# Optimization experiments

Hardware: AMD Instinct MI355X
Metric: run time of the kernel (lower is better)

The kernel has to match this reference:

```python
import jax, jax.numpy as jnp
import numpy as np

D_MODEL = 1024
N_HEADS = 16
N_KV_HEADS = 4
HEAD_DIM = D_MODEL // N_HEADS
GROUP = N_HEADS // N_KV_HEADS
ROPE_BASE = 10000.0


def _rope(x):
    # x: (B, H, T, Dh); standard rotate-half RoPE, base 10000
    B, H, T, Dh = x.shape
    inv_freq = 1.0 / (ROPE_BASE ** (jnp.arange(0, Dh, 2, dtype=jnp.float32) / Dh))
    t = jnp.arange(T, dtype=jnp.float32)
    freqs = t[:, None] * inv_freq[None, :]              # (T, Dh/2)
    emb = jnp.concatenate([freqs, freqs], axis=-1)      # (T, Dh)
    cos = jnp.cos(emb)[None, None].astype(x.dtype)
    sin = jnp.sin(emb)[None, None].astype(x.dtype)
    x1, x2 = x[..., : Dh // 2], x[..., Dh // 2 :]
    rot = jnp.concatenate([-x2, x1], axis=-1)
    return x * cos + rot * sin


def setup_inputs() -> dict:
    key = jax.random.key(0)
    ks = jax.random.split(key, 5)
    B, T = 2, 2048
    s = 1.0 / np.sqrt(D_MODEL)
    return {
        "x": jax.random.normal(ks[0], (B, T, D_MODEL), dtype=jnp.float32),
        "wq": jax.random.normal(ks[1], (D_MODEL, N_HEADS * HEAD_DIM), dtype=jnp.float32) * s,
        "wk": jax.random.normal(ks[2], (D_MODEL, N_KV_HEADS * HEAD_DIM), dtype=jnp.float32) * s,
        "wv": jax.random.normal(ks[3], (D_MODEL, N_KV_HEADS * HEAD_DIM), dtype=jnp.float32) * s,
        "wo": jax.random.normal(ks[4], (N_HEADS * HEAD_DIM, D_MODEL), dtype=jnp.float32) * s,
    }


def reference(x, wq, wk, wv, wo):
    B, T, _ = x.shape
    q = (x @ wq).reshape(B, T, N_HEADS, HEAD_DIM).transpose(0, 2, 1, 3)      # (B,H,T,Dh)
    k = (x @ wk).reshape(B, T, N_KV_HEADS, HEAD_DIM).transpose(0, 2, 1, 3)   # (B,Hk,T,Dh)
    v = (x @ wv).reshape(B, T, N_KV_HEADS, HEAD_DIM).transpose(0, 2, 1, 3)
    q = _rope(q)
    k = _rope(k)
    # repeat_interleave kv heads group_size times -> (B, H, T, Dh)
    k = jnp.repeat(k, GROUP, axis=1)
    v = jnp.repeat(v, GROUP, axis=1)
    scale = 1.0 / np.sqrt(HEAD_DIM)
    scores = jnp.einsum("bhqd,bhkd->bhqk", q, k) * scale                      # (B,H,T,T)
    causal = jnp.tril(jnp.ones((T, T), dtype=bool))
    scores = jnp.where(causal[None, None], scores, -jnp.inf)
    attn = jax.nn.softmax(scores, axis=-1)
    out = jnp.einsum("bhqk,bhkd->bhqd", attn, v)                              # (B,H,T,Dh)
    out = out.transpose(0, 2, 1, 3).reshape(B, T, N_HEADS * HEAD_DIM)
    return out @ wo
```

## Files before the change

kernel.cpp:

```cpp
#include <hip/hip_runtime.h>

typedef short bshort8 __attribute__((ext_vector_type(8)));
typedef float f32x4 __attribute__((ext_vector_type(4)));

#define DEVFN static __device__ __forceinline__

DEVFN unsigned short f2bf(float f) {
    union { float f; unsigned u; } v; v.f = f;
    unsigned r = (v.u + 0x7FFFu + ((v.u >> 16) & 1u)) >> 16;
    return (unsigned short)r;
}

DEVFN float bf2f(unsigned short u) {
    union { unsigned u; float f; } v; v.u = (unsigned)u << 16;
    return v.f;
}

DEVFN unsigned cvt_pk_bf16(float a, float b) {
    unsigned r;
    asm("v_cvt_pk_bf16_f32 %0, %1, %2" : "=v"(r) : "v"(a), "v"(b));
    return r;
}

DEVFN float exp2_fast(float x) {
    float r;
    asm("v_exp_f32 %0, %1" : "=v"(r) : "v"(x));
    return r;
}

DEVFN int swzf(int row) { return (row & 7) ^ ((row >> 3) & 7); }
DEVFN int swzf2(int row) { return (row & 3) ^ ((row >> 2) & 3); }

#define GLDS16(g, l)                                                            \
    __builtin_amdgcn_global_load_lds(                                           \
        (__attribute__((address_space(1))) void*)(g),                           \
        (__attribute__((address_space(3))) void*)(l), 16, 0, 0)

__global__ void prep_kernel(const float* __restrict__ x,
                            const float* __restrict__ wq,
                            const float* __restrict__ wk,
                            const float* __restrict__ wv,
                            const float* __restrict__ wo,
                            unsigned short* __restrict__ xb,
                            unsigned short* __restrict__ wt,
                            unsigned short* __restrict__ wot,
                            float2* __restrict__ cs) {
    const int z = blockIdx.z;
    int tx = threadIdx.x, ty = threadIdx.y;
    if (z >= 5) {
        int i = ((z - 5) * 1024 + blockIdx.y * 32 + blockIdx.x) * 256 + ty * 32 + tx;
        float4 v = ((const float4*)x)[i];
        ushort4 o;
        o.x = f2bf(v.x); o.y = f2bf(v.y); o.z = f2bf(v.z); o.w = f2bf(v.w);
        ((ushort4*)xb)[i] = o;
        return;
    }
    if (z == 4) {
        int idx = (blockIdx.y * 32 + blockIdx.x) * 256 + ty * 32 + tx;
        if (idx < 65536) {
            int t = idx >> 5, i = idx & 31;
            float inv_freq = powf(10000.0f, -(float)i / 32.0f);
            float a = (float)t * inv_freq;
            cs[idx] = make_float2(cosf(a), sinf(a));
        }
        return;
    }
    const float* src;
    unsigned short* dst;
    int N;
    if (z == 0)      { src = wq; dst = wt;                N = 1024; }
    else if (z == 1) { src = wk; dst = wt + 1024 * 1024;  N = 256; }
    else if (z == 2) { src = wv; dst = wt + 1280 * 1024;  N = 256; }
    else             { src = wo; dst = wot;               N = 1024; }
    if (blockIdx.x * 32 >= N) return;
    __shared__ float tile[32][33];
    int n0 = blockIdx.x * 32, k0 = blockIdx.y * 32;
#pragma unroll
    for (int i = 0; i < 4; i++)
        tile[ty + i * 8][tx] = src[(size_t)(k0 + ty + i * 8) * N + n0 + tx];
    __syncthreads();
#pragma unroll
    for (int i = 0; i < 4; i++)
        dst[(size_t)(n0 + ty + i * 8) * 1024 + k0 + tx] = f2bf(tile[tx][ty + i * 8]);
}


__global__ __launch_bounds__(256) void gemm_qkv_kernel(
    const unsigned short* __restrict__ xb, const unsigned short* __restrict__ wt,
    const float2* __restrict__ cs, unsigned short* __restrict__ Qb,
    unsigned short* __restrict__ Kb, unsigned short* __restrict__ Vt) {
    __shared__ char smem[49152];
    const int tid = threadIdx.x;
    const int lane = tid & 63, w = tid >> 6;
    const int m0 = blockIdx.y * 128, n0 = blockIdx.x * 64;
    const int l15 = lane & 15, g = lane >> 4;
    const int l8 = lane >> 3, c8 = lane & 7;

    const unsigned short* srcA[4];
    int dstA[4];
#pragma unroll
    for (int j = 0; j < 4; j++) {
        int row = w * 32 + j * 8 + l8;
        srcA[j] = xb + (size_t)(m0 + row) * 1024 + (c8 ^ swzf(row)) * 8;
        dstA[j] = w * 4096 + j * 1024 + lane * 16;
    }
    const unsigned short* srcB[2];
    int dstB[2];
#pragma unroll
    for (int j = 0; j < 2; j++) {
        int row = w * 16 + j * 8 + l8;
        srcB[j] = wt + (size_t)(n0 + row) * 1024 + (c8 ^ swzf(row)) * 8;
        dstB[j] = 0x8000 + w * 2048 + j * 1024 + lane * 16;
    }

    int aOff[2][2], bOff[4][2];
#pragma unroll
    for (int fm = 0; fm < 2; fm++) {
        int row = w * 32 + fm * 16 + l15;
#pragma unroll
        for (int ks = 0; ks < 2; ks++)
            aOff[fm][ks] = row * 128 + (((ks * 4 + g) ^ swzf(row)) << 4);
    }
#pragma unroll
    for (int fn = 0; fn < 4; fn++) {
        int row = fn * 16 + l15;
#pragma unroll
        for (int ks = 0; ks < 2; ks++)
            bOff[fn][ks] = row * 128 + (((ks * 4 + g) ^ swzf(row)) << 4);
    }

    f32x4 acc[2][4] = {};
#pragma unroll
    for (int j = 0; j < 4; j++) GLDS16(srcA[j], smem + dstA[j]);
#pragma unroll
    for (int j = 0; j < 2; j++) GLDS16(srcB[j], smem + dstB[j]);
    asm volatile("s_waitcnt vmcnt(0)" ::: "memory");
    __builtin_amdgcn_s_barrier();

    for (int kt = 0; kt < 16; kt++) {
        const int curA = (kt & 1) << 14;
        const int curB = (kt & 1) << 13;
        if (kt < 15) {
            const int nA = curA ^ 0x4000, nB = curB ^ 0x2000;
#pragma unroll
            for (int j = 0; j < 4; j++)
                GLDS16(srcA[j] + (kt + 1) * 64, smem + nA + dstA[j]);
#pragma unroll
            for (int j = 0; j < 2; j++)
                GLDS16(srcB[j] + (kt + 1) * 64, smem + nB + dstB[j]);
        }
        bshort8 af[2][2], bf[4][2];
#pragma unroll
        for (int fm = 0; fm < 2; fm++)
#pragma unroll
            for (int ks = 0; ks < 2; ks++)
                af[fm][ks] = *(const bshort8*)(smem + curA + aOff[fm][ks]);
#pragma unroll
        for (int fn = 0; fn < 4; fn++)
#pragma unroll
            for (int ks = 0; ks < 2; ks++)
                bf[fn][ks] = *(const bshort8*)(smem + 0x8000 + curB + bOff[fn][ks]);
        asm volatile("s_waitcnt lgkmcnt(0)" ::: "memory");
        __builtin_amdgcn_sched_barrier(0);
#pragma unroll
        for (int fm = 0; fm < 2; fm++)
#pragma unroll
            for (int fn = 0; fn < 4; fn++) {
                acc[fm][fn] = __builtin_amdgcn_mfma_f32_16x16x32_bf16(
                    af[fm][0], bf[fn][0], acc[fm][fn], 0, 0, 0);
                acc[fm][fn] = __builtin_amdgcn_mfma_f32_16x16x32_bf16(
                    af[fm][1], bf[fn][1], acc[fm][fn], 0, 0, 0);
            }
        if (kt < 15) {
            asm volatile("s_waitcnt vmcnt(0)" ::: "memory");
            __builtin_amdgcn_s_barrier();
        }
    }

    const bool isV = (n0 >= 1280);
    const bool isK = (n0 >= 1024) && !isV;
#pragma unroll
    for (int fm = 0; fm < 2; fm++) {
#pragma unroll
        for (int r = 0; r < 4; r++) {
            int m = m0 + w * 32 + fm * 16 + g * 4 + r;
            int b = m >> 11, t = m & 2047;
            if (isV) {
#pragma unroll
                for (int fn = 0; fn < 4; fn++) {
                    int n = n0 + fn * 16 + l15;
                    int d = n & 63, vh = (n - 1280) >> 6;
                    Vt[((size_t)(b * 4 + vh) * 64 + d) * 2048 + t] =
                        f2bf(acc[fm][fn][r]);
                }
            } else {
                float2 c0 = cs[t * 32 + l15];
                float2 c1 = cs[t * 32 + 16 + l15];
#pragma unroll
                for (int fn = 0; fn < 4; fn++) {
                    int n = n0 + fn * 16 + l15;
                    int d = n & 63;
                    float val = acc[fm][fn][r];
                    float pair = acc[fm][fn ^ 2][r];
                    float rot = (fn < 2) ? -pair : pair;
                    float2 cc = (fn & 1) ? c1 : c0;
                    float o = val * cc.x + rot * cc.y;
                    if (isK) {
                        int kh = (n - 1024) >> 6;
                        Kb[((size_t)(b * 4 + kh) * 2048 + t) * 64 + d] = f2bf(o);
                    } else {
                        o *= 0.1803368801111504f;
                        int h = n >> 6;
                        Qb[((size_t)(b * 16 + h) * 2048 + t) * 64 + d] = f2bf(o);
                    }
                }
            }
        }
    }
}


__global__ __launch_bounds__(256) void attn_kernel(
    const unsigned short* __restrict__ Qb, const unsigned short* __restrict__ Kb,
    const unsigned short* __restrict__ Vt, unsigned short* __restrict__ Opart,
    float* __restrict__ ml) {
    __shared__ char smem[24576];
    const int tid = threadIdx.x, lane = tid & 63, w = tid >> 6;
    const int l15 = lane & 15, g = lane >> 4;
    const int id = blockIdx.x;
    const int grp = id & 7;
    const int b = grp >> 2, kvh = grp & 3;
    const int i = id >> 3;
    const int hh = i & 3;
    const int h = kvh * 4 + hh;
    const int c = 79 - (i >> 2);
    int qt, s;
    if (c < 8)       { qt = c;                    s = 0; }
    else if (c < 24) { qt = 8 + ((c - 8) >> 1);   s = (c - 8) & 1; }
    else if (c < 48) { qt = 16 + (c - 24) / 3;    s = (c - 24) % 3; }
    else             { qt = 24 + ((c - 48) >> 2); s = (c - 48) & 3; }
    const int k0t = s * 8;
    const int nk = min(8, qt + 1 - k0t);
    const int qs = qt * 64;
    const int slot = (b * 16 + h) * 80 + c;

    const unsigned short* Kbase = Kb + (size_t)(b * 4 + kvh) * 2048 * 64;
    const unsigned short* Vbase = Vt + (size_t)(b * 4 + kvh) * 64 * 2048;
    const unsigned short* Qhead = Qb + (size_t)(b * 16 + h) * 2048 * 64;

    const int srow8 = lane >> 3;
    const int sci = lane & 7;
    const int sk = (l15 & 7) ^ (l15 >> 3);
    const int strip = w * 2048;

    const int rowb = l15 * 128 + ((g ^ sk) << 4);
    int Akn[4];
#pragma unroll
    for (int fn = 0; fn < 4; fn++) {
        int nr = ((fn >> 1) << 5) + ((l15 >> 2) << 3) + ((fn & 1) << 2) + (l15 & 3);
        int key = (nr & 7) ^ ((nr >> 3) & 1);
        Akn[fn] = nr * 128 + ((g ^ key) << 4);
    }

    const int lc0 = sci ^ srow8;
    const int lc1 = sci ^ srow8 ^ 1;
    const int r0 = w * 16 + srow8, r1 = w * 16 + 8 + srow8;
    const int kdst = strip + lane * 16;
    const int vdst0 = 0x2000 + strip + lane * 16;

    const unsigned short* Qrow = Qhead + (size_t)(qs + w * 16 + l15) * 64 + g * 8;
    bshort8 qf0 = *(const bshort8*)(Qrow);
    bshort8 qf1 = *(const bshort8*)(Qrow + 32);

    GLDS16(Kbase + (size_t)(k0t * 64 + r0) * 64 + lc0 * 8, smem + kdst);
    GLDS16(Kbase + (size_t)(k0t * 64 + r1) * 64 + lc1 * 8, smem + kdst + 1024);
    GLDS16(Vbase + (size_t)r0 * 2048 + k0t * 64 + lc0 * 8, smem + vdst0);
    GLDS16(Vbase + (size_t)r1 * 2048 + k0t * 64 + lc1 * 8, smem + vdst0 + 1024);
    __syncthreads();

    bshort8 ones;
#pragma unroll
    for (int j = 0; j < 8; j++) ones[j] = (short)0x3F80;

    const unsigned short* gk0 = Kbase + (size_t)((k0t + 1) * 64 + r0) * 64 + lc0 * 8;
    const unsigned short* gk1 = Kbase + (size_t)((k0t + 1) * 64 + r1) * 64 + lc1 * 8;
    const unsigned short* gv0 = Vbase + (size_t)r0 * 2048 + (k0t + 1) * 64 + lc0 * 8;
    const unsigned short* gv1 = Vbase + (size_t)r1 * 2048 + (k0t + 1) * 64 + lc1 * 8;

    f32x4 l_acc = {};
    f32x4 O[4] = {};
    const int qlocal = w * 16 + l15;
    const bool has_diag = (k0t + nk - 1 == qt);

    auto body = [&](int kt, bool more) {
        const int vb = (kt & 1) ? 0x4000 : 0x2000;
        const int vnb = (kt & 1) ? 0x2000 : 0x4000;
        if (more) {
            GLDS16(gv0 + kt * 64, smem + vnb + strip + lane * 16);
            GLDS16(gv1 + kt * 64, smem + vnb + strip + lane * 16 + 1024);
        }
        f32x4 S[4];
        __builtin_amdgcn_s_setprio(1);
#pragma unroll
        for (int fn = 0; fn < 4; fn++) {
            bshort8 k0 = *(const bshort8*)(smem + Akn[fn]);
            bshort8 k1 = *(const bshort8*)(smem + (Akn[fn] ^ 0x40));
            f32x4 a = {};
            a = __builtin_amdgcn_mfma_f32_16x16x32_bf16(k0, qf0, a, 0, 0, 0);
            a = __builtin_amdgcn_mfma_f32_16x16x32_bf16(k1, qf1, a, 0, 0, 0);
            S[fn] = a;
        }
        __builtin_amdgcn_s_setprio(0);
        __builtin_amdgcn_s_barrier();
        if (more) {
            GLDS16(gk0 + (size_t)kt * 4096, smem + kdst);
            GLDS16(gk1 + (size_t)kt * 4096, smem + kdst + 1024);
        }
        if (has_diag && !more) {
#pragma unroll
            for (int fn = 0; fn < 4; fn++)
#pragma unroll
                for (int r = 0; r < 4; r++) {
                    int kvl = ((fn >> 1) << 5) + (g << 3) + ((fn & 1) << 2) + r;
                    if (kvl > qlocal) S[fn][r] = -1e30f;
                }
        }
        float p[4][4];
#pragma unroll
        for (int fn = 0; fn < 4; fn++)
#pragma unroll
            for (int r = 0; r < 4; r++) p[fn][r] = exp2_fast(S[fn][r]);
        union PF { unsigned d[4]; bshort8 v; };
        PF u0, u1;
        u0.d[0] = cvt_pk_bf16(p[0][0], p[0][1]);
        u0.d[1] = cvt_pk_bf16(p[0][2], p[0][3]);
        u0.d[2] = cvt_pk_bf16(p[1][0], p[1][1]);
        u0.d[3] = cvt_pk_bf16(p[1][2], p[1][3]);
        u1.d[0] = cvt_pk_bf16(p[2][0], p[2][1]);
        u1.d[1] = cvt_pk_bf16(p[2][2], p[2][3]);
        u1.d[2] = cvt_pk_bf16(p[3][0], p[3][1]);
        u1.d[3] = cvt_pk_bf16(p[3][2], p[3][3]);
        __builtin_amdgcn_s_setprio(1);
        l_acc = __builtin_amdgcn_mfma_f32_16x16x32_bf16(ones, u0.v, l_acc, 0, 0, 0);
        l_acc = __builtin_amdgcn_mfma_f32_16x16x32_bf16(ones, u1.v, l_acc, 0, 0, 0);
#pragma unroll
        for (int fd = 0; fd < 4; fd++) {
            bshort8 v0 = *(const bshort8*)(smem + vb + rowb + fd * 2048);
            bshort8 v1 = *(const bshort8*)(smem + ((vb + rowb + fd * 2048) ^ 64));
            O[fd] = __builtin_amdgcn_mfma_f32_16x16x32_bf16(v0, u0.v, O[fd], 0, 0, 0);
            O[fd] = __builtin_amdgcn_mfma_f32_16x16x32_bf16(v1, u1.v, O[fd], 0, 0, 0);
        }
        __builtin_amdgcn_s_setprio(0);
        if (more) __syncthreads();
    };

    if (nk == 8) {
#pragma unroll
        for (int kt = 0; kt < 8; kt++) body(kt, kt < 7);
    } else {
        for (int kt = 0; kt < nk; kt++) body(kt, kt < nk - 1);
    }

    __syncthreads();
    if (g == 0) {
        ml[(size_t)slot * 64 + w * 16 + l15] = l_acc[0];
    }
#pragma unroll
    for (int fd = 0; fd < 4; fd++)
#pragma unroll
        for (int w2 = 0; w2 < 2; w2++) {
            unsigned word = cvt_pk_bf16(O[fd][2 * w2], O[fd][2 * w2 + 1]);
            int byte = fd * 32 + g * 8 + w2 * 4;
            *(unsigned*)(smem + strip + l15 * 128 + (((byte >> 4) ^ sk) << 4) +
                         (byte & 15)) = word;
        }
    asm volatile("s_waitcnt lgkmcnt(0)" ::: "memory");
    __builtin_amdgcn_sched_barrier(0);
#pragma unroll
    for (int it = 0; it < 2; it++) {
        int r16 = it * 8 + srow8;
        int4 vv = *(const int4*)(smem + strip + r16 * 128 +
                                 ((sci ^ srow8 ^ it) << 4));
        *(int4*)(Opart + (size_t)slot * 4096 + (w * 16 + r16) * 64 + sci * 8) = vv;
    }
}

__global__ __launch_bounds__(256) void combine_kernel(
    const unsigned short* __restrict__ Opart, const float* __restrict__ ml,
    unsigned short* __restrict__ Ob) {
    const int qt = blockIdx.x, h = blockIdx.y, b = blockIdx.z;
    const int S = (qt >> 3) + 1;
    int c0;
    if (qt < 8)       c0 = qt;
    else if (qt < 16) c0 = 8 + (qt - 8) * 2;
    else if (qt < 24) c0 = 24 + (qt - 16) * 3;
    else              c0 = 48 + (qt - 24) * 4;
    const int slotbase = (b * 16 + h) * 80 + c0;
    const int t = threadIdx.x;
    const int q = t >> 2, dq = (t & 3) * 16;

    float L = 0.f;
#pragma unroll
    for (int i = 0; i < 4; i++)
        if (i < S) L += ml[(size_t)(slotbase + i) * 64 + q];

    float acc[16] = {};
#pragma unroll
    for (int i = 0; i < 4; i++) {
        if (i < S) {
            const unsigned short* P =
                Opart + (size_t)(slotbase + i) * 4096 + q * 64 + dq;
            int4 a0 = *(const int4*)P;
            int4 a1 = *(const int4*)(P + 8);
            unsigned u[8] = {(unsigned)a0.x, (unsigned)a0.y, (unsigned)a0.z,
                             (unsigned)a0.w, (unsigned)a1.x, (unsigned)a1.y,
                             (unsigned)a1.z, (unsigned)a1.w};
#pragma unroll
            for (int j = 0; j < 8; j++) {
                acc[2 * j]     += bf2f((unsigned short)(u[j] & 0xFFFF));
                acc[2 * j + 1] += bf2f((unsigned short)(u[j] >> 16));
            }
        }
    }
    float invL = 1.0f / L;
    int4 o0, o1;
    o0.x = cvt_pk_bf16(acc[0] * invL, acc[1] * invL);
    o0.y = cvt_pk_bf16(acc[2] * invL, acc[3] * invL);
    o0.z = cvt_pk_bf16(acc[4] * invL, acc[5] * invL);
    o0.w = cvt_pk_bf16(acc[6] * invL, acc[7] * invL);
    o1.x = cvt_pk_bf16(acc[8] * invL, acc[9] * invL);
    o1.y = cvt_pk_bf16(acc[10] * invL, acc[11] * invL);
    o1.z = cvt_pk_bf16(acc[12] * invL, acc[13] * invL);
    o1.w = cvt_pk_bf16(acc[14] * invL, acc[15] * invL);
    unsigned short* dst =
        Ob + (size_t)(b * 2048 + qt * 64 + q) * 1024 + h * 64 + dq;
    *(int4*)dst = o0;
    *(int4*)(dst + 8) = o1;
}

__global__ __launch_bounds__(256) void gemm_out_kernel(
    const unsigned short* __restrict__ ab, const unsigned short* __restrict__ wot,
    float* __restrict__ out) {
    __shared__ char smem[49152];
    const int tid = threadIdx.x;
    const int lane = tid & 63, w = tid >> 6;
    const int m0 = blockIdx.y * 128, n0 = blockIdx.x * 64;
    const int l15 = lane & 15, g = lane >> 4;
    const int l8 = lane >> 3, c8 = lane & 7;

    const unsigned short* srcA[4];
    int dstA[4];
#pragma unroll
    for (int j = 0; j < 4; j++) {
        int row = w * 32 + j * 8 + l8;
        srcA[j] = ab + (size_t)(m0 + row) * 1024 + (c8 ^ swzf(row)) * 8;
        dstA[j] = w * 4096 + j * 1024 + lane * 16;
    }
    const unsigned short* srcB[2];
    int dstB[2];
#pragma unroll
    for (int j = 0; j < 2; j++) {
        int row = w * 16 + j * 8 + l8;
        srcB[j] = wot + (size_t)(n0 + row) * 1024 + (c8 ^ swzf(row)) * 8;
        dstB[j] = 0x8000 + w * 2048 + j * 1024 + lane * 16;
    }

    int aOff[2][2], bOff[4][2];
#pragma unroll
    for (int fm = 0; fm < 2; fm++) {
        int row = w * 32 + fm * 16 + l15;
#pragma unroll
        for (int ks = 0; ks < 2; ks++)
            aOff[fm][ks] = row * 128 + (((ks * 4 + g) ^ swzf(row)) << 4);
    }
#pragma unroll
    for (int fn = 0; fn < 4; fn++) {
        int row = fn * 16 + l15;
#pragma unroll
        for (int ks = 0; ks < 2; ks++)
            bOff[fn][ks] = row * 128 + (((ks * 4 + g) ^ swzf(row)) << 4);
    }

    f32x4 acc[2][4] = {};
#pragma unroll
    for (int j = 0; j < 4; j++) GLDS16(srcA[j], smem + dstA[j]);
#pragma unroll
    for (int j = 0; j < 2; j++) GLDS16(srcB[j], smem + dstB[j]);
    asm volatile("s_waitcnt vmcnt(0)" ::: "memory");
    __builtin_amdgcn_s_barrier();

    for (int kt = 0; kt < 16; kt++) {
        const int curA = (kt & 1) << 14;
        const int curB = (kt & 1) << 13;
        if (kt < 15) {
            const int nA = curA ^ 0x4000, nB = curB ^ 0x2000;
#pragma unroll
            for (int j = 0; j < 4; j++)
                GLDS16(srcA[j] + (kt + 1) * 64, smem + nA + dstA[j]);
#pragma unroll
            for (int j = 0; j < 2; j++)
                GLDS16(srcB[j] + (kt + 1) * 64, smem + nB + dstB[j]);
        }
        bshort8 af[2][2], bf[4][2];
#pragma unroll
        for (int fm = 0; fm < 2; fm++)
#pragma unroll
            for (int ks = 0; ks < 2; ks++)
                af[fm][ks] = *(const bshort8*)(smem + curA + aOff[fm][ks]);
#pragma unroll
        for (int fn = 0; fn < 4; fn++)
#pragma unroll
            for (int ks = 0; ks < 2; ks++)
                bf[fn][ks] = *(const bshort8*)(smem + 0x8000 + curB + bOff[fn][ks]);
        asm volatile("s_waitcnt lgkmcnt(0)" ::: "memory");
        __builtin_amdgcn_sched_barrier(0);
#pragma unroll
        for (int fm = 0; fm < 2; fm++)
#pragma unroll
            for (int fn = 0; fn < 4; fn++) {
                acc[fm][fn] = __builtin_amdgcn_mfma_f32_16x16x32_bf16(
                    af[fm][0], bf[fn][0], acc[fm][fn], 0, 0, 0);
                acc[fm][fn] = __builtin_amdgcn_mfma_f32_16x16x32_bf16(
                    af[fm][1], bf[fn][1], acc[fm][fn], 0, 0, 0);
            }
        if (kt < 15) {
            asm volatile("s_waitcnt vmcnt(0)" ::: "memory");
            __builtin_amdgcn_s_barrier();
        }
    }
#pragma unroll
    for (int fm = 0; fm < 2; fm++)
#pragma unroll
        for (int r = 0; r < 4; r++) {
            int m = m0 + w * 32 + fm * 16 + g * 4 + r;
#pragma unroll
            for (int fn = 0; fn < 4; fn++) {
                int n = n0 + fn * 16 + l15;
                out[(size_t)m * 1024 + n] = acc[fm][fn][r];
            }
        }
}


extern "C" void kernel_launch(void* const* d_in, const int* in_sizes, int n_in,
                              void* d_out, int out_size, void* d_ws, size_t ws_size,
                              hipStream_t stream) {
    const float* x = (const float*)d_in[0];
    const float* wq = (const float*)d_in[1];
    const float* wk = (const float*)d_in[2];
    const float* wv = (const float*)d_in[3];
    const float* wo = (const float*)d_in[4];
    float* out = (float*)d_out;
    char* ws = (char*)d_ws;

    unsigned short* xb = (unsigned short*)(ws);
    unsigned short* wt = (unsigned short*)(ws + 8388608);
    float* ml = (float*)(ws + 8388608);
    unsigned short* wot = (unsigned short*)(ws + 11534336);
    float2* cs = (float2*)(ws + 13631488);
    unsigned short* Qb = (unsigned short*)(ws + 14155776);
    unsigned short* Kb = (unsigned short*)(ws + 22544384);
    unsigned short* Vtr = (unsigned short*)(ws + 26738688);
    unsigned short* Opart = (unsigned short*)(ws + 28835840);
    unsigned short* Ob = xb;

    hipLaunchKernelGGL(prep_kernel, dim3(32, 32, 9), dim3(32, 8), 0, stream, x,
                       wq, wk, wv, wo, xb, wt, wot, cs);
    hipLaunchKernelGGL(gemm_qkv_kernel, dim3(24, 32), dim3(256), 0, stream, xb, wt,
                       cs, Qb, Kb, Vtr);
    hipLaunchKernelGGL(attn_kernel, dim3(2560), dim3(256), 0, stream, Qb, Kb,
                       Vtr, Opart, ml);
    hipLaunchKernelGGL(combine_kernel, dim3(32, 16, 2), dim3(256), 0, stream,
                       Opart, ml, Ob);
    hipLaunchKernelGGL(gemm_out_kernel, dim3(16, 32), dim3(256), 0, stream, Ob,
                       wot, out);
}
```

Measured before the change: 86.58 us.

## Double-buffer K tiles in attention and write single-split tiles directly to output

```diff
diff --git a/kernel.cpp b/kernel.cpp
--- a/kernel.cpp
+++ b/kernel.cpp
@@ -223,8 +223,8 @@
 __global__ __launch_bounds__(256) void attn_kernel(
     const unsigned short* __restrict__ Qb, const unsigned short* __restrict__ Kb,
     const unsigned short* __restrict__ Vt, unsigned short* __restrict__ Opart,
-    float* __restrict__ ml) {
-    __shared__ char smem[24576];
+    float* __restrict__ ml, unsigned short* __restrict__ Ob) {
+    __shared__ char smem[32768];
     const int tid = threadIdx.x, lane = tid & 63, w = tid >> 6;
     const int l15 = lane & 15, g = lane >> 4;
     const int id = blockIdx.x;
@@ -265,17 +265,17 @@
     const int lc0 = sci ^ srow8;
     const int lc1 = sci ^ srow8 ^ 1;
     const int r0 = w * 16 + srow8, r1 = w * 16 + 8 + srow8;
-    const int kdst = strip + lane * 16;
-    const int vdst0 = 0x2000 + strip + lane * 16;
+    const int kdst_off = strip + lane * 16;
 
     const unsigned short* Qrow = Qhead + (size_t)(qs + w * 16 + l15) * 64 + g * 8;
     bshort8 qf0 = *(const bshort8*)(Qrow);
     bshort8 qf1 = *(const bshort8*)(Qrow + 32);
 
-    GLDS16(Kbase + (size_t)(k0t * 64 + r0) * 64 + lc0 * 8, smem + kdst);
-    GLDS16(Kbase + (size_t)(k0t * 64 + r1) * 64 + lc1 * 8, smem + kdst + 1024);
-    GLDS16(Vbase + (size_t)r0 * 2048 + k0t * 64 + lc0 * 8, smem + vdst0);
-    GLDS16(Vbase + (size_t)r1 * 2048 + k0t * 64 + lc1 * 8, smem + vdst0 + 1024);
+    GLDS16(Kbase + (size_t)(k0t * 64 + r0) * 64 + lc0 * 8, smem + kdst_off);
+    GLDS16(Kbase + (size_t)(k0t * 64 + r1) * 64 + lc1 * 8, smem + kdst_off + 1024);
+    GLDS16(Vbase + (size_t)r0 * 2048 + k0t * 64 + lc0 * 8, smem + 0x4000 + kdst_off);
+    GLDS16(Vbase + (size_t)r1 * 2048 + k0t * 64 + lc1 * 8,
+           smem + 0x4000 + kdst_off + 1024);
     __syncthreads();
 
     bshort8 ones;
@@ -293,29 +293,26 @@
     const bool has_diag = (k0t + nk - 1 == qt);
 
     auto body = [&](int kt, bool more) {
-        const int vb = (kt & 1) ? 0x4000 : 0x2000;
-        const int vnb = (kt & 1) ? 0x2000 : 0x4000;
+        const int kb = (kt & 1) ? 0x2000 : 0x0000;
+        const int vb = (kt & 1) ? 0x6000 : 0x4000;
         if (more) {
-            GLDS16(gv0 + kt * 64, smem + vnb + strip + lane * 16);
-            GLDS16(gv1 + kt * 64, smem + vnb + strip + lane * 16 + 1024);
+            GLDS16(gk0 + (size_t)kt * 4096, smem + (kb ^ 0x2000) + kdst_off);
+            GLDS16(gk1 + (size_t)kt * 4096, smem + (kb ^ 0x2000) + kdst_off + 1024);
+            GLDS16(gv0 + kt * 64, smem + (vb ^ 0x2000) + kdst_off);
+            GLDS16(gv1 + kt * 64, smem + (vb ^ 0x2000) + kdst_off + 1024);
         }
         f32x4 S[4];
         __builtin_amdgcn_s_setprio(1);
 #pragma unroll
         for (int fn = 0; fn < 4; fn++) {
-            bshort8 k0 = *(const bshort8*)(smem + Akn[fn]);
-            bshort8 k1 = *(const bshort8*)(smem + (Akn[fn] ^ 0x40));
+            bshort8 k0 = *(const bshort8*)(smem + kb + Akn[fn]);
+            bshort8 k1 = *(const bshort8*)(smem + kb + (Akn[fn] ^ 0x40));
             f32x4 a = {};
             a = __builtin_amdgcn_mfma_f32_16x16x32_bf16(k0, qf0, a, 0, 0, 0);
             a = __builtin_amdgcn_mfma_f32_16x16x32_bf16(k1, qf1, a, 0, 0, 0);
             S[fn] = a;
         }
         __builtin_amdgcn_s_setprio(0);
-        __builtin_amdgcn_s_barrier();
-        if (more) {
-            GLDS16(gk0 + (size_t)kt * 4096, smem + kdst);
-            GLDS16(gk1 + (size_t)kt * 4096, smem + kdst + 1024);
-        }
         if (has_diag && !more) {
 #pragma unroll
             for (int fn = 0; fn < 4; fn++)
@@ -362,14 +359,17 @@
     }
 
     __syncthreads();
-    if (g == 0) {
+    const bool direct = (c < 8);
+    const float scale = direct ? (1.0f / l_acc[0]) : 1.0f;
+    if (!direct && g == 0) {
         ml[(size_t)slot * 64 + w * 16 + l15] = l_acc[0];
     }
 #pragma unroll
     for (int fd = 0; fd < 4; fd++)
 #pragma unroll
         for (int w2 = 0; w2 < 2; w2++) {
-            unsigned word = cvt_pk_bf16(O[fd][2 * w2], O[fd][2 * w2 + 1]);
+            unsigned word =
+                cvt_pk_bf16(O[fd][2 * w2] * scale, O[fd][2 * w2 + 1] * scale);
             int byte = fd * 32 + g * 8 + w2 * 4;
             *(unsigned*)(smem + strip + l15 * 128 + (((byte >> 4) ^ sk) << 4) +
                          (byte & 15)) = word;
@@ -381,18 +381,23 @@
         int r16 = it * 8 + srow8;
         int4 vv = *(const int4*)(smem + strip + r16 * 128 +
                                  ((sci ^ srow8 ^ it) << 4));
-        *(int4*)(Opart + (size_t)slot * 4096 + (w * 16 + r16) * 64 + sci * 8) = vv;
+        if (direct) {
+            *(int4*)(Ob + (size_t)(b * 2048 + qs + w * 16 + r16) * 1024 + h * 64 +
+                     sci * 8) = vv;
+        } else {
+            *(int4*)(Opart + (size_t)slot * 4096 + (w * 16 + r16) * 64 + sci * 8) =
+                vv;
+        }
     }
 }
 
 __global__ __launch_bounds__(256) void combine_kernel(
     const unsigned short* __restrict__ Opart, const float* __restrict__ ml,
     unsigned short* __restrict__ Ob) {
-    const int qt = blockIdx.x, h = blockIdx.y, b = blockIdx.z;
+    const int qt = 8 + blockIdx.x, h = blockIdx.y, b = blockIdx.z;
     const int S = (qt >> 3) + 1;
     int c0;
-    if (qt < 8)       c0 = qt;
-    else if (qt < 16) c0 = 8 + (qt - 8) * 2;
+    if (qt < 16)      c0 = 8 + (qt - 8) * 2;
     else if (qt < 24) c0 = 24 + (qt - 16) * 3;
     else              c0 = 48 + (qt - 24) * 4;
     const int slotbase = (b * 16 + h) * 80 + c0;
@@ -569,8 +574,8 @@
     hipLaunchKernelGGL(gemm_qkv_kernel, dim3(24, 32), dim3(256), 0, stream, xb, wt,
                        cs, Qb, Kb, Vtr);
     hipLaunchKernelGGL(attn_kernel, dim3(2560), dim3(256), 0, stream, Qb, Kb,
-                       Vtr, Opart, ml);
-    hipLaunchKernelGGL(combine_kernel, dim3(32, 16, 2), dim3(256), 0, stream,
+                       Vtr, Opart, ml, Ob);
+    hipLaunchKernelGGL(combine_kernel, dim3(24, 16, 2), dim3(256), 0, stream,
                        Opart, ml, Ob);
     hipLaunchKernelGGL(gemm_out_kernel, dim3(16, 32), dim3(256), 0, stream, Ob,
                        wot, out);
```

Result: no change. 85.71 us (median of 3 runs) (-1.0%).
